# Kernel tuning notes

Measured on AMD Instinct MI355X. Metric: run time of the kernel, lower is better.

The kernel has to match this reference:

```python
import jax, jax.numpy as jnp
import numpy as np

B, N, D = 16, 2048, 128  # batch, nodes, embedding_dim

def setup_inputs() -> dict:
    key = jax.random.key(0)
    ks = jax.random.split(key, 12)
    def dense(kw, kb, din, dout):
        # keras Dense default glorot_uniform weight, zeros bias (use small random bias for generality)
        lim = np.sqrt(6.0 / (din + dout))
        W = jax.random.uniform(kw, (din, dout), minval=-lim, maxval=lim, dtype=jnp.float32)
        b = jax.random.normal(kb, (dout,), dtype=jnp.float32) * 0.01
        return W, b
    Wq, bq = dense(ks[0], ks[1], D, D)
    Wk, bk = dense(ks[2], ks[3], D, D)
    Wv, bv = dense(ks[4], ks[5], D, D)
    Wo, bo = dense(ks[6], ks[7], D, D)
    query_ = jax.random.normal(ks[8], (B, N, D), dtype=jnp.float32)
    key_ = jax.random.normal(ks[9], (B, N, D), dtype=jnp.float32)
    mask = jax.random.randint(ks[10], (B, N + 1, N + 1), 0, 2).astype(bool)
    return {"query_": query_, "key_": key_, "mask": mask,
            "Wq": Wq, "bq": bq, "Wk": Wk, "bk": bk,
            "Wv": Wv, "bv": bv, "Wo": Wo, "bo": bo}

def reference(query_, key_, mask, Wq, bq, Wk, bk, Wv, bv, Wo, bo):
    q = query_ @ Wq + bq                       # [B,N,D]
    k = key_ @ Wk + bk                         # [B,N,D]
    comp = jnp.einsum('bqd,bkd->bqk', q, k)    # [B,N,N]
    comp = comp / jnp.sqrt(jnp.asarray(k.shape[-1], jnp.float32))
    m = mask[:, 1:, 1:]                        # [B,N,N]
    comp = jnp.where(m, -jnp.inf, comp)
    attn = jax.nn.softmax(comp, axis=-1)
    attn = jnp.where(jnp.isnan(attn), 0.0, attn)  # fully-masked rows -> 0
    # NOTE: faithful to source: value projection applied to the PROJECTED key
    v = k @ Wv + bv                            # [B,N,D]
    out = jnp.einsum('bqk,bkd->bqd', attn, v)
    return out @ Wo + bo
```

## Files before the change

### kernel.cpp

```cpp
#include <hip/hip_runtime.h>

#define SB 16
#define SN 2048
#define SD 128
#define NM 2049
#define SZ (SB*SN*SD)

typedef __bf16 bf16x8 __attribute__((ext_vector_type(8)));
typedef float f32x4 __attribute__((ext_vector_type(4)));

__device__ __forceinline__ unsigned short f2b(float f){
  union { float f; unsigned int u; } v; v.f = f;
  unsigned int r = v.u + 0x7fffu + ((v.u >> 16) & 1u);
  return (unsigned short)(r >> 16);
}

__device__ __forceinline__ void async16(const void* g, void* l){
  __builtin_amdgcn_global_load_lds(
      (__attribute__((address_space(1))) void*)(g),
      (__attribute__((address_space(3))) void*)(l), 16, 0, 0);
}

__global__ __launch_bounds__(256) void prep_w_kernel(
    const float* __restrict__ Wq, const float* __restrict__ Wk,
    const float* __restrict__ Wv, const float* __restrict__ Wo,
    unsigned short* __restrict__ out)
{
  int widx = blockIdx.x >> 4;
  int kg   = blockIdx.x & 15;
  const float* W = (widx==0)?Wq:(widx==1)?Wk:(widx==2)?Wv:Wo;
  unsigned short* O = out + widx*16384;
  int t = threadIdx.x;
  int k = kg*8 + (t>>5);
  int n = (t&31)*4;
  float4 v = *reinterpret_cast<const float4*>(W + k*SD + n);
  O[(n+0)*SD + k] = f2b(v.x);
  O[(n+1)*SD + k] = f2b(v.y);
  O[(n+2)*SD + k] = f2b(v.z);
  O[(n+3)*SD + k] = f2b(v.w);
}

__global__ __launch_bounds__(256,4) void qkv_kernel(
    const float* __restrict__ query, const float* __restrict__ key,
    const unsigned short* __restrict__ wts,
    const float* __restrict__ bq, const float* __restrict__ bk,
    const float* __restrict__ bv,
    unsigned short* __restrict__ qb, unsigned short* __restrict__ kb,
    unsigned short* __restrict__ vt)
{
  __shared__ unsigned short kstrip[2][16*136];
  __shared__ unsigned short vT[SD*40];

  int tid=threadIdx.x;
  int w=tid>>6, ln=tid&63, g=ln>>4, lm=ln&15;
  int b = blockIdx.x >> 6, nt = blockIdx.x & 63;
  int n0 = nt*32;
  size_t rowbase = (size_t)b*SN + n0;
  const float sc = 0.08838834764831845f;

  const unsigned short* WqT = wts;
  const unsigned short* WkT = wts + 16384;
  const unsigned short* WvT = wts + 32768;

  if (w < 2){
    const float* xr = query + (rowbase + w*16 + lm)*SD;
    bf16x8 af[4];
    for (int ks=0;ks<4;ks++){
      float4 x0 = *reinterpret_cast<const float4*>(xr + ks*32 + g*8);
      float4 x1 = *reinterpret_cast<const float4*>(xr + ks*32 + g*8 + 4);
      union { bf16x8 v; unsigned short s[8]; } u;
      u.s[0]=f2b(x0.x); u.s[1]=f2b(x0.y); u.s[2]=f2b(x0.z); u.s[3]=f2b(x0.w);
      u.s[4]=f2b(x1.x); u.s[5]=f2b(x1.y); u.s[6]=f2b(x1.z); u.s[7]=f2b(x1.w);
      af[ks]=u.v;
    }
    for (int d=0; d<8; d++){
      f32x4 acc = {0.f,0.f,0.f,0.f};
      for (int ks=0;ks<4;ks++){
        bf16x8 wf = *reinterpret_cast<const bf16x8*>(WqT + (d*16+lm)*SD + ks*32 + g*8);
        acc = __builtin_amdgcn_mfma_f32_16x16x32_bf16(af[ks], wf, acc, 0,0,0);
      }
      float bb = bq[d*16+lm];
      for (int r=0;r<4;r++)
        qb[(rowbase + w*16 + 4*g + r)*SD + d*16 + lm] = f2b((acc[r]+bb)*sc);
    }
  } else {
    int wv = w-2;
    const float* xr = key + (rowbase + wv*16 + lm)*SD;
    bf16x8 af[4];
    for (int ks=0;ks<4;ks++){
      float4 x0 = *reinterpret_cast<const float4*>(xr + ks*32 + g*8);
      float4 x1 = *reinterpret_cast<const float4*>(xr + ks*32 + g*8 + 4);
      union { bf16x8 v; unsigned short s[8]; } u;
      u.s[0]=f2b(x0.x); u.s[1]=f2b(x0.y); u.s[2]=f2b(x0.z); u.s[3]=f2b(x0.w);
      u.s[4]=f2b(x1.x); u.s[5]=f2b(x1.y); u.s[6]=f2b(x1.z); u.s[7]=f2b(x1.w);
      af[ks]=u.v;
    }
    unsigned short* ks_ = kstrip[wv];
    for (int d=0; d<8; d++){
      f32x4 acc = {0.f,0.f,0.f,0.f};
      for (int ks=0;ks<4;ks++){
        bf16x8 wf = *reinterpret_cast<const bf16x8*>(WkT + (d*16+lm)*SD + ks*32 + g*8);
        acc = __builtin_amdgcn_mfma_f32_16x16x32_bf16(af[ks], wf, acc, 0,0,0);
      }
      float bb = bk[d*16+lm];
      for (int r=0;r<4;r++){
        unsigned short kv = f2b(acc[r]+bb);
        kb[(rowbase + wv*16 + 4*g + r)*SD + d*16 + lm] = kv;
        ks_[(4*g+r)*136 + d*16 + lm] = kv;
      }
    }
    bf16x8 ka[4];
    for (int ks=0;ks<4;ks++)
      ka[ks] = *reinterpret_cast<const bf16x8*>(&ks_[lm*136 + ks*32 + g*8]);
    for (int d=0; d<8; d++){
      f32x4 acc = {0.f,0.f,0.f,0.f};
      for (int ks=0;ks<4;ks++){
        bf16x8 wf = *reinterpret_cast<const bf16x8*>(WvT + (d*16+lm)*SD + ks*32 + g*8);
        acc = __builtin_amdgcn_mfma_f32_16x16x32_bf16(ka[ks], wf, acc, 0,0,0);
      }
      float bb = bv[d*16+lm];
      ushort4 pk;
      pk.x=f2b(acc[0]+bb); pk.y=f2b(acc[1]+bb);
      pk.z=f2b(acc[2]+bb); pk.w=f2b(acc[3]+bb);
      *reinterpret_cast<ushort4*>(&vT[(d*16+lm)*40 + wv*16 + 4*g]) = pk;
    }
  }
  __syncthreads();
  int d = tid>>1, half = tid&1;
  const uint4* src = reinterpret_cast<const uint4*>(&vT[d*40 + half*16]);
  uint4* dst = reinterpret_cast<uint4*>(vt + (size_t)b*SD*SN + (size_t)d*SN + n0 + half*16);
  dst[0]=src[0]; dst[1]=src[1];
}

__global__ __launch_bounds__(256,4) void flash_kernel(
    const unsigned short* __restrict__ qb, const unsigned short* __restrict__ kb,
    const unsigned short* __restrict__ vt, const int* __restrict__ mask,
    const unsigned short* __restrict__ WoT, const float* __restrict__ bo,
    float* __restrict__ out)
{
  __shared__ unsigned short bufK[2][64*128];
  __shared__ unsigned short bufV[2][128*64];
  __shared__ unsigned short ldsP[4*16*72];

  int tid=threadIdx.x;
  int w=tid>>6, ln=tid&63, g=ln>>4, lm=ln&15;
  int b = blockIdx.x >> 5, qt = blockIdx.x & 31;
  int q0 = qt*64;

  const unsigned short* Qb = qb + (size_t)b*SN*SD;
  const unsigned short* Kb = kb + (size_t)b*SN*SD;
  const unsigned short* Vb = vt + (size_t)b*SD*SN;
  const int* Mb = mask + (size_t)b*NM*NM;

  auto issueK = [&](int k0, int bi){
    const char* gbase = (const char*)Kb + (size_t)k0*256;
    for (int c=0;c<4;c++){
      int p = c*256 + tid;
      int row = p>>4, lc = (p&15) ^ (row&15);
      async16(gbase + (size_t)row*256 + lc*16, (char*)bufK[bi] + p*16);
    }
  };
  auto issueV = [&](int k0, int bi){
    const char* gbase = (const char*)Vb + (size_t)k0*2;
    for (int c=0;c<4;c++){
      int p = c*256 + tid;
      int row = p>>3, lc = (p&7) ^ (row&7);
      async16(gbase + (size_t)row*4096 + lc*16, (char*)bufV[bi] + p*16);
    }
  };

  issueK(0,0); issueV(0,0);

  bf16x8 qf[4];
  {
    const unsigned short* qr = Qb + (size_t)(q0 + w*16 + lm)*SD;
    for (int ks=0;ks<4;ks++)
      qf[ks] = *reinterpret_cast<const bf16x8*>(qr + ks*32 + g*8);
  }

  int qr1 = 1 + q0 + w*16 + 4*g;
  const int* mbase = Mb + (size_t)qr1*NM + 1 + lm;
  int mreg[16];
  for (int ct=0;ct<4;ct++)
    for (int r=0;r<4;r++)
      mreg[ct*4+r] = mbase[(size_t)r*NM + ct*16];

  float mrow[4], lrow[4], al[4];
  f32x4 acc[8];
  for (int r=0;r<4;r++){ mrow[r]=-INFINITY; lrow[r]=0.f; }
  for (int d=0;d<8;d++){ f32x4 z={0.f,0.f,0.f,0.f}; acc[d]=z; }
  unsigned short* pw = &ldsP[w*16*72];

  for (int kt=0; kt<32; kt++){
    __syncthreads();
    int cur = kt&1;
    if (kt<31){ issueK((kt+1)*64, cur^1); issueV((kt+1)*64, cur^1); }

    f32x4 s[4];
    for (int ct=0;ct<4;ct++){
      f32x4 z = {0.f,0.f,0.f,0.f};
      for (int ks=0;ks<4;ks++){
        bf16x8 kf = *reinterpret_cast<const bf16x8*>(
            &bufK[cur][(ct*16+lm)*128 + (((ks*4+g)^lm))*8]);
        z = __builtin_amdgcn_mfma_f32_16x16x32_bf16(qf[ks], kf, z, 0,0,0);
      }
      s[ct]=z;
    }

    for (int ct=0;ct<4;ct++)
      for (int r=0;r<4;r++)
        s[ct][r] = mreg[ct*4+r] ? -INFINITY : s[ct][r];
    if (kt<31){
      const int* mp = mbase + (kt+1)*64;
      for (int ct=0;ct<4;ct++)
        for (int r=0;r<4;r++)
          mreg[ct*4+r] = mp[(size_t)r*NM + ct*16];
    }

    for (int r=0;r<4;r++){
      float v = fmaxf(fmaxf(s[0][r],s[1][r]), fmaxf(s[2][r],s[3][r]));
      v = fmaxf(v, __shfl_xor(v,1,16));
      v = fmaxf(v, __shfl_xor(v,2,16));
      v = fmaxf(v, __shfl_xor(v,4,16));
      v = fmaxf(v, __shfl_xor(v,8,16));
      float mn = fmaxf(mrow[r], v);
      bool dead = (mn == -INFINITY);
      float a = dead ? 1.f : __expf(mrow[r]-mn);
      float rsum = 0.f;
      for (int ct=0;ct<4;ct++){
        float p = dead ? 0.f : __expf(s[ct][r]-mn);
        s[ct][r]=p; rsum += p;
      }
      rsum += __shfl_xor(rsum,1,16);
      rsum += __shfl_xor(rsum,2,16);
      rsum += __shfl_xor(rsum,4,16);
      rsum += __shfl_xor(rsum,8,16);
      lrow[r] = lrow[r]*a + rsum;
      mrow[r] = mn;
      al[r] = a;
    }
    for (int d=0;d<8;d++)
      for (int r=0;r<4;r++)
        acc[d][r] *= al[r];

    for (int ct=0;ct<4;ct++){
      int col = ct*16+lm;
      for (int r=0;r<4;r++)
        pw[(4*g+r)*72 + col] = f2b(s[ct][r]);
    }
    bf16x8 pa0 = *reinterpret_cast<const bf16x8*>(&pw[lm*72 + g*8]);
    bf16x8 pa1 = *reinterpret_cast<const bf16x8*>(&pw[lm*72 + 32 + g*8]);

    for (int d=0;d<8;d++){
      bf16x8 v0 = *reinterpret_cast<const bf16x8*>(
          &bufV[cur][(d*16+lm)*64 + ((g^(lm&7)))*8]);
      acc[d] = __builtin_amdgcn_mfma_f32_16x16x32_bf16(pa0, v0, acc[d], 0,0,0);
      bf16x8 v1 = *reinterpret_cast<const bf16x8*>(
          &bufV[cur][(d*16+lm)*64 + (((4+g)^(lm&7)))*8]);
      acc[d] = __builtin_amdgcn_mfma_f32_16x16x32_bf16(pa1, v1, acc[d], 0,0,0);
    }
  }

  __syncthreads();
  float inv[4];
  for (int r=0;r<4;r++) inv[r] = (lrow[r] > 0.f) ? (1.f/lrow[r]) : 0.f;
  unsigned short* strip = &bufK[0][0] + w*2176;
  for (int d=0;d<8;d++)
    for (int r=0;r<4;r++)
      strip[(4*g+r)*136 + d*16 + lm] = f2b(acc[d][r]*inv[r]);
  bf16x8 oa[4];
  for (int ks=0;ks<4;ks++)
    oa[ks] = *reinterpret_cast<const bf16x8*>(&strip[lm*136 + ks*32 + g*8]);
  float* Ob = out + ((size_t)b*SN + q0 + w*16)*SD;
  for (int dc=0; dc<8; dc++){
    f32x4 o = {0.f,0.f,0.f,0.f};
    for (int ks=0;ks<4;ks++){
      bf16x8 wf = *reinterpret_cast<const bf16x8*>(WoT + (dc*16+lm)*SD + ks*32 + g*8);
      o = __builtin_amdgcn_mfma_f32_16x16x32_bf16(oa[ks], wf, o, 0,0,0);
    }
    float bb = bo[dc*16+lm];
    for (int r=0;r<4;r++)
      Ob[(size_t)(4*g+r)*SD + dc*16 + lm] = o[r]+bb;
  }
}

extern "C" void kernel_launch(void* const* d_in, const int* in_sizes, int n_in,
                              void* d_out, int out_size, void* d_ws, size_t ws_size,
                              hipStream_t stream)
{
  const float* query = (const float*)d_in[0];
  const float* key   = (const float*)d_in[1];
  const int*   mask  = (const int*)d_in[2];
  const float* Wq = (const float*)d_in[3];
  const float* bq = (const float*)d_in[4];
  const float* Wk = (const float*)d_in[5];
  const float* bk = (const float*)d_in[6];
  const float* Wv = (const float*)d_in[7];
  const float* bv = (const float*)d_in[8];
  const float* Wo = (const float*)d_in[9];
  const float* bo = (const float*)d_in[10];
  float* out = (float*)d_out;

  unsigned short* qb = (unsigned short*)d_ws;
  unsigned short* kb = qb + SZ;
  unsigned short* vt = kb + SZ;
  unsigned short* wts = vt + SZ;

  prep_w_kernel<<<64,256,0,stream>>>(Wq,Wk,Wv,Wo,wts);
  qkv_kernel  <<<1024,256,0,stream>>>(query, key, wts, bq, bk, bv, qb, kb, vt);
  flash_kernel<<<512,256,0,stream>>>(qb, kb, vt, mask, wts+49152, bo, out);
}
```

Baseline: 490.7 us.

## Pre-pack mask into bitmasks and stage QKV weights in LDS

Adds a pre-pass that converts the int32 mask into 64-bit ballot bitmasks per row and key tile, so the flash kernel reads one 8-byte word per row per tile instead of sixteen scattered int loads. The QKV kernel is restructured to split Q and K/V blocks, stage the bf16 weight matrices in padded LDS, and write V transposed in wider chunks. Probabilities use a cheaper round-to-nearest bf16 conversion. This trades an extra full pass over the mask for smaller, coalesced mask reads inside the attention loop, and it uses more LDS per block in the QKV kernel.

```diff
diff --git a/kernel.cpp b/kernel.cpp
--- a/kernel.cpp
+++ b/kernel.cpp
@@ -5,6 +5,7 @@
 #define SD 128
 #define NM 2049
 #define SZ (SB*SN*SD)
+#define WLDS 17408
 
 typedef __bf16 bf16x8 __attribute__((ext_vector_type(8)));
 typedef float f32x4 __attribute__((ext_vector_type(4)));
@@ -14,6 +15,10 @@
   unsigned int r = v.u + 0x7fffu + ((v.u >> 16) & 1u);
   return (unsigned short)(r >> 16);
 }
+__device__ __forceinline__ unsigned short f2b_fast(float f){
+  union { float f; unsigned int u; } v; v.f = f;
+  return (unsigned short)((v.u + 0x8000u) >> 16);
+}
 
 __device__ __forceinline__ void async16(const void* g, void* l){
   __builtin_amdgcn_global_load_lds(
@@ -21,26 +26,52 @@
       (__attribute__((address_space(3))) void*)(l), 16, 0, 0);
 }
 
-__global__ __launch_bounds__(256) void prep_w_kernel(
+__global__ __launch_bounds__(256) void prep_pack_kernel(
     const float* __restrict__ Wq, const float* __restrict__ Wk,
     const float* __restrict__ Wv, const float* __restrict__ Wo,
-    unsigned short* __restrict__ out)
+    const int* __restrict__ mask,
+    unsigned short* __restrict__ wts, unsigned long long* __restrict__ pm)
 {
-  int widx = blockIdx.x >> 4;
-  int kg   = blockIdx.x & 15;
-  const float* W = (widx==0)?Wq:(widx==1)?Wk:(widx==2)?Wv:Wo;
-  unsigned short* O = out + widx*16384;
-  int t = threadIdx.x;
-  int k = kg*8 + (t>>5);
-  int n = (t&31)*4;
-  float4 v = *reinterpret_cast<const float4*>(W + k*SD + n);
-  O[(n+0)*SD + k] = f2b(v.x);
-  O[(n+1)*SD + k] = f2b(v.y);
-  O[(n+2)*SD + k] = f2b(v.z);
-  O[(n+3)*SD + k] = f2b(v.w);
-}
-
-__global__ __launch_bounds__(256,4) void qkv_kernel(
+  if (blockIdx.x < 64){
+    int widx = blockIdx.x >> 4;
+    int kg   = blockIdx.x & 15;
+    const float* W = (widx==0)?Wq:(widx==1)?Wk:(widx==2)?Wv:Wo;
+    unsigned short* O = wts + widx*16384;
+    int t = threadIdx.x;
+    int k = kg*8 + (t>>5);
+    int n = (t&31)*4;
+    float4 v = *reinterpret_cast<const float4*>(W + k*SD + n);
+    O[(n+0)*SD + k] = f2b(v.x);
+    O[(n+1)*SD + k] = f2b(v.y);
+    O[(n+2)*SD + k] = f2b(v.z);
+    O[(n+3)*SD + k] = f2b(v.w);
+    return;
+  }
+  int widx = blockIdx.x - 64;
+  int wave = widx*4 + (threadIdx.x>>6);
+  int ln = threadIdx.x & 63;
+  size_t wb0 = (size_t)wave*256;
+  for (int rr=0; rr<32; rr++){
+    size_t wb = wb0 + rr*8;
+    int v[8];
+    for (int i=0;i<8;i++){
+      size_t wbi = wb + i;
+      int bb = (int)(wbi>>16); int rem = (int)(wbi & 65535);
+      int row = rem>>5; int kt = rem&31;
+      v[i] = mask[(size_t)bb*NM*NM + (size_t)(row+1)*NM + 1 + kt*64 + ln];
+    }
+    unsigned long long bt[8];
+    for (int i=0;i<8;i++) bt[i] = __ballot(v[i]!=0);
+    if (ln==0){
+      for (int i=0;i<4;i++){
+        ulonglong2 t; t.x = bt[2*i]; t.y = bt[2*i+1];
+        *reinterpret_cast<ulonglong2*>(&pm[wb + 2*i]) = t;
+      }
+    }
+  }
+}
+
+__global__ __launch_bounds__(256) void qkv_kernel(
     const float* __restrict__ query, const float* __restrict__ key,
     const unsigned short* __restrict__ wts,
     const float* __restrict__ bq, const float* __restrict__ bk,
@@ -48,22 +79,25 @@
     unsigned short* __restrict__ qb, unsigned short* __restrict__ kb,
     unsigned short* __restrict__ vt)
 {
-  __shared__ unsigned short kstrip[2][16*136];
-  __shared__ unsigned short vT[SD*40];
-
+  __shared__ unsigned short lds[2*WLDS + 9216];
   int tid=threadIdx.x;
   int w=tid>>6, ln=tid&63, g=ln>>4, lm=ln&15;
-  int b = blockIdx.x >> 6, nt = blockIdx.x & 63;
-  int n0 = nt*32;
-  size_t rowbase = (size_t)b*SN + n0;
+  bool isq = blockIdx.x < 512;
+  int id = isq ? blockIdx.x : (blockIdx.x - 512);
+  int bb = id>>5, n0 = (id&31)*64;
+  size_t rowbase = (size_t)bb*SN + n0 + w*16;
   const float sc = 0.08838834764831845f;
 
-  const unsigned short* WqT = wts;
-  const unsigned short* WkT = wts + 16384;
-  const unsigned short* WvT = wts + 32768;
-
-  if (w < 2){
-    const float* xr = query + (rowbase + w*16 + lm)*SD;
+  if (isq){
+    for (int i=0;i<8;i++){
+      int p = i*256+tid; int row=p>>4, c=p&15;
+      uint4 t = *reinterpret_cast<const uint4*>(wts + p*8);
+      *reinterpret_cast<uint4*>(&lds[row*136 + c*8]) = t;
+    }
+    __syncthreads();
+    float bqv[8];
+    for (int d=0;d<8;d++) bqv[d] = bq[d*16+lm];
+    const float* xr = query + (rowbase + lm)*SD;
     bf16x8 af[4];
     for (int ks=0;ks<4;ks++){
       float4 x0 = *reinterpret_cast<const float4*>(xr + ks*32 + g*8);
@@ -76,16 +110,27 @@
     for (int d=0; d<8; d++){
       f32x4 acc = {0.f,0.f,0.f,0.f};
       for (int ks=0;ks<4;ks++){
-        bf16x8 wf = *reinterpret_cast<const bf16x8*>(WqT + (d*16+lm)*SD + ks*32 + g*8);
+        bf16x8 wf = *reinterpret_cast<const bf16x8*>(&lds[(d*16+lm)*136 + ks*32 + g*8]);
         acc = __builtin_amdgcn_mfma_f32_16x16x32_bf16(af[ks], wf, acc, 0,0,0);
       }
-      float bb = bq[d*16+lm];
       for (int r=0;r<4;r++)
-        qb[(rowbase + w*16 + 4*g + r)*SD + d*16 + lm] = f2b((acc[r]+bb)*sc);
+        qb[(rowbase + 4*g + r)*SD + d*16 + lm] = f2b((acc[r]+bqv[d])*sc);
     }
   } else {
-    int wv = w-2;
-    const float* xr = key + (rowbase + wv*16 + lm)*SD;
+    for (int i=0;i<8;i++){
+      int p = i*256+tid; int row=p>>4, c=p&15;
+      uint4 t = *reinterpret_cast<const uint4*>(wts + 16384 + p*8);
+      *reinterpret_cast<uint4*>(&lds[row*136 + c*8]) = t;
+    }
+    for (int i=0;i<8;i++){
+      int p = i*256+tid; int row=p>>4, c=p&15;
+      uint4 t = *reinterpret_cast<const uint4*>(wts + 32768 + p*8);
+      *reinterpret_cast<uint4*>(&lds[WLDS + row*136 + c*8]) = t;
+    }
+    __syncthreads();
+    float bkv[8], bvv[8];
+    for (int d=0;d<8;d++){ bkv[d]=bk[d*16+lm]; bvv[d]=bv[d*16+lm]; }
+    const float* xr = key + (rowbase + lm)*SD;
     bf16x8 af[4];
     for (int ks=0;ks<4;ks++){
       float4 x0 = *reinterpret_cast<const float4*>(xr + ks*32 + g*8);
@@ -95,46 +140,47 @@
       u.s[4]=f2b(x1.x); u.s[5]=f2b(x1.y); u.s[6]=f2b(x1.z); u.s[7]=f2b(x1.w);
       af[ks]=u.v;
     }
-    unsigned short* ks_ = kstrip[wv];
+    unsigned short* strip = &lds[2*WLDS + w*2176];
     for (int d=0; d<8; d++){
       f32x4 acc = {0.f,0.f,0.f,0.f};
       for (int ks=0;ks<4;ks++){
-        bf16x8 wf = *reinterpret_cast<const bf16x8*>(WkT + (d*16+lm)*SD + ks*32 + g*8);
+        bf16x8 wf = *reinterpret_cast<const bf16x8*>(&lds[(d*16+lm)*136 + ks*32 + g*8]);
         acc = __builtin_amdgcn_mfma_f32_16x16x32_bf16(af[ks], wf, acc, 0,0,0);
       }
-      float bb = bk[d*16+lm];
       for (int r=0;r<4;r++){
-        unsigned short kv = f2b(acc[r]+bb);
-        kb[(rowbase + wv*16 + 4*g + r)*SD + d*16 + lm] = kv;
-        ks_[(4*g+r)*136 + d*16 + lm] = kv;
+        unsigned short kv2 = f2b(acc[r]+bkv[d]);
+        kb[(rowbase + 4*g + r)*SD + d*16 + lm] = kv2;
+        strip[(4*g+r)*136 + d*16 + lm] = kv2;
       }
     }
     bf16x8 ka[4];
     for (int ks=0;ks<4;ks++)
-      ka[ks] = *reinterpret_cast<const bf16x8*>(&ks_[lm*136 + ks*32 + g*8]);
+      ka[ks] = *reinterpret_cast<const bf16x8*>(&strip[lm*136 + ks*32 + g*8]);
+    __syncthreads();
+    unsigned short* vT = &lds[2*WLDS];
     for (int d=0; d<8; d++){
       f32x4 acc = {0.f,0.f,0.f,0.f};
       for (int ks=0;ks<4;ks++){
-        bf16x8 wf = *reinterpret_cast<const bf16x8*>(WvT + (d*16+lm)*SD + ks*32 + g*8);
+        bf16x8 wf = *reinterpret_cast<const bf16x8*>(&lds[WLDS + (d*16+lm)*136 + ks*32 + g*8]);
         acc = __builtin_amdgcn_mfma_f32_16x16x32_bf16(ka[ks], wf, acc, 0,0,0);
       }
-      float bb = bv[d*16+lm];
       ushort4 pk;
-      pk.x=f2b(acc[0]+bb); pk.y=f2b(acc[1]+bb);
-      pk.z=f2b(acc[2]+bb); pk.w=f2b(acc[3]+bb);
-      *reinterpret_cast<ushort4*>(&vT[(d*16+lm)*40 + wv*16 + 4*g]) = pk;
-    }
-  }
-  __syncthreads();
-  int d = tid>>1, half = tid&1;
-  const uint4* src = reinterpret_cast<const uint4*>(&vT[d*40 + half*16]);
-  uint4* dst = reinterpret_cast<uint4*>(vt + (size_t)b*SD*SN + (size_t)d*SN + n0 + half*16);
-  dst[0]=src[0]; dst[1]=src[1];
+      pk.x=f2b(acc[0]+bvv[d]); pk.y=f2b(acc[1]+bvv[d]);
+      pk.z=f2b(acc[2]+bvv[d]); pk.w=f2b(acc[3]+bvv[d]);
+      *reinterpret_cast<ushort4*>(&vT[(d*16+lm)*72 + w*16 + 4*g]) = pk;
+    }
+    __syncthreads();
+    for (int i=0;i<4;i++){
+      int idx = i*256+tid; int row = idx>>3, c8 = idx&7;
+      uint4 t = *reinterpret_cast<const uint4*>(&vT[row*72 + c8*8]);
+      *reinterpret_cast<uint4*>(vt + (size_t)bb*SD*SN + (size_t)row*SN + n0 + c8*8) = t;
+    }
+  }
 }
 
 __global__ __launch_bounds__(256,4) void flash_kernel(
     const unsigned short* __restrict__ qb, const unsigned short* __restrict__ kb,
-    const unsigned short* __restrict__ vt, const int* __restrict__ mask,
+    const unsigned short* __restrict__ vt, const unsigned long long* __restrict__ pm,
     const unsigned short* __restrict__ WoT, const float* __restrict__ bo,
     float* __restrict__ out)
 {
@@ -150,7 +196,6 @@
   const unsigned short* Qb = qb + (size_t)b*SN*SD;
   const unsigned short* Kb = kb + (size_t)b*SN*SD;
   const unsigned short* Vb = vt + (size_t)b*SD*SN;
-  const int* Mb = mask + (size_t)b*NM*NM;
 
   auto issueK = [&](int k0, int bi){
     const char* gbase = (const char*)Kb + (size_t)k0*256;
@@ -178,12 +223,9 @@
       qf[ks] = *reinterpret_cast<const bf16x8*>(qr + ks*32 + g*8);
   }
 
-  int qr1 = 1 + q0 + w*16 + 4*g;
-  const int* mbase = Mb + (size_t)qr1*NM + 1 + lm;
-  int mreg[16];
-  for (int ct=0;ct<4;ct++)
-    for (int r=0;r<4;r++)
-      mreg[ct*4+r] = mbase[(size_t)r*NM + ct*16];
+  const unsigned long long* pmr = pm + ((size_t)b*SN + q0 + w*16 + 4*g)*32;
+  unsigned long long pmc[4];
+  for (int r=0;r<4;r++) pmc[r] = pmr[(size_t)r*32];
 
   float mrow[4], lrow[4], al[4];
   f32x4 acc[8];
@@ -207,15 +249,17 @@
       s[ct]=z;
     }
 
-    for (int ct=0;ct<4;ct++)
-      for (int r=0;r<4;r++)
-        s[ct][r] = mreg[ct*4+r] ? -INFINITY : s[ct][r];
-    if (kt<31){
-      const int* mp = mbase + (kt+1)*64;
-      for (int ct=0;ct<4;ct++)
-        for (int r=0;r<4;r++)
-          mreg[ct*4+r] = mp[(size_t)r*NM + ct*16];
-    }
+    for (int r=0;r<4;r++){
+      unsigned int lo = (unsigned int)pmc[r];
+      unsigned int hi = (unsigned int)(pmc[r]>>32);
+      unsigned int l = lo >> lm, h = hi >> lm;
+      if (l & 1u)       s[0][r] = -INFINITY;
+      if (l & 0x10000u) s[1][r] = -INFINITY;
+      if (h & 1u)       s[2][r] = -INFINITY;
+      if (h & 0x10000u) s[3][r] = -INFINITY;
+    }
+    if (kt<31)
+      for (int r=0;r<4;r++) pmc[r] = pmr[(size_t)r*32 + kt + 1];
 
     for (int r=0;r<4;r++){
       float v = fmaxf(fmaxf(s[0][r],s[1][r]), fmaxf(s[2][r],s[3][r]));
@@ -246,7 +290,7 @@
     for (int ct=0;ct<4;ct++){
       int col = ct*16+lm;
       for (int r=0;r<4;r++)
-        pw[(4*g+r)*72 + col] = f2b(s[ct][r]);
+        pw[(4*g+r)*72 + col] = f2b_fast(s[ct][r]);
     }
     bf16x8 pa0 = *reinterpret_cast<const bf16x8*>(&pw[lm*72 + g*8]);
     bf16x8 pa1 = *reinterpret_cast<const bf16x8*>(&pw[lm*72 + 32 + g*8]);
@@ -305,8 +349,9 @@
   unsigned short* kb = qb + SZ;
   unsigned short* vt = kb + SZ;
   unsigned short* wts = vt + SZ;
-
-  prep_w_kernel<<<64,256,0,stream>>>(Wq,Wk,Wv,Wo,wts);
-  qkv_kernel  <<<1024,256,0,stream>>>(query, key, wts, bq, bk, bv, qb, kb, vt);
-  flash_kernel<<<512,256,0,stream>>>(qb, kb, vt, mask, wts+49152, bo, out);
-}
+  unsigned long long* pm = (unsigned long long*)(wts + 65536);
+
+  prep_pack_kernel<<<1088,256,0,stream>>>(Wq,Wk,Wv,Wo, mask, wts, pm);
+  qkv_kernel      <<<1024,256,0,stream>>>(query, key, wts, bq, bk, bv, qb, kb, vt);
+  flash_kernel    <<<512,256,0,stream>>>(qb, kb, vt, pm, wts+49152, bo, out);
+}
```

After: 519.7 us. +5.9%, slower.

## Pack int mask into bitmask in projection kernel; coalesce Q/K stores via LDS

Applied to the files above, without the earlier changes.

Adds 1024 extra blocks to the QKV projection kernel that read the int32 mask and ballot it into 64-bit bitmasks, one word per row per 64-column tile. The flash kernel then loads only these packed bits instead of strided int32 mask reads in its inner loop. Q and K outputs are now staged through LDS and written as 16-byte vectors, and P uses a cheaper rounding conversion. The mask still has to be read once in full, plus a write and re-read of the packed form, and the cheaper rounding slightly changes how ties round.

```diff
diff --git a/kernel.cpp b/kernel.cpp
--- a/kernel.cpp
+++ b/kernel.cpp
@@ -14,6 +14,10 @@
   unsigned int r = v.u + 0x7fffu + ((v.u >> 16) & 1u);
   return (unsigned short)(r >> 16);
 }
+__device__ __forceinline__ unsigned short f2b_fast(float f){
+  union { float f; unsigned int u; } v; v.f = f;
+  return (unsigned short)((v.u + 0x8000u) >> 16);
+}
 
 __device__ __forceinline__ void async16(const void* g, void* l){
   __builtin_amdgcn_global_load_lds(
@@ -24,117 +28,141 @@
 __global__ __launch_bounds__(256) void prep_w_kernel(
     const float* __restrict__ Wq, const float* __restrict__ Wk,
     const float* __restrict__ Wv, const float* __restrict__ Wo,
-    unsigned short* __restrict__ out)
+    unsigned short* __restrict__ wts)
 {
-  int widx = blockIdx.x >> 4;
-  int kg   = blockIdx.x & 15;
-  const float* W = (widx==0)?Wq:(widx==1)?Wk:(widx==2)?Wv:Wo;
-  unsigned short* O = out + widx*16384;
-  int t = threadIdx.x;
-  int k = kg*8 + (t>>5);
-  int n = (t&31)*4;
-  float4 v = *reinterpret_cast<const float4*>(W + k*SD + n);
-  O[(n+0)*SD + k] = f2b(v.x);
-  O[(n+1)*SD + k] = f2b(v.y);
-  O[(n+2)*SD + k] = f2b(v.z);
-  O[(n+3)*SD + k] = f2b(v.w);
-}
-
-__global__ __launch_bounds__(256,4) void qkv_kernel(
+  int widx=blockIdx.x>>4, kg=blockIdx.x&15;
+  const float* W=(widx==0)?Wq:(widx==1)?Wk:(widx==2)?Wv:Wo;
+  unsigned short* O=wts+widx*16384;
+  int t=threadIdx.x;
+  int k=kg*8+(t>>5), n=(t&31)*4;
+  float4 v=*reinterpret_cast<const float4*>(W+k*SD+n);
+  O[(n+0)*SD+k]=f2b(v.x); O[(n+1)*SD+k]=f2b(v.y);
+  O[(n+2)*SD+k]=f2b(v.z); O[(n+3)*SD+k]=f2b(v.w);
+}
+
+__global__ __launch_bounds__(256) void combo_kernel(
     const float* __restrict__ query, const float* __restrict__ key,
+    const int* __restrict__ mask,
     const unsigned short* __restrict__ wts,
     const float* __restrict__ bq, const float* __restrict__ bk,
     const float* __restrict__ bv,
     unsigned short* __restrict__ qb, unsigned short* __restrict__ kb,
-    unsigned short* __restrict__ vt)
+    unsigned short* __restrict__ vt, unsigned long long* __restrict__ pm)
 {
-  __shared__ unsigned short kstrip[2][16*136];
-  __shared__ unsigned short vT[SD*40];
-
+  __shared__ unsigned short smem[13824];
   int tid=threadIdx.x;
   int w=tid>>6, ln=tid&63, g=ln>>4, lm=ln&15;
-  int b = blockIdx.x >> 6, nt = blockIdx.x & 63;
-  int n0 = nt*32;
-  size_t rowbase = (size_t)b*SN + n0;
-  const float sc = 0.08838834764831845f;
-
-  const unsigned short* WqT = wts;
-  const unsigned short* WkT = wts + 16384;
-  const unsigned short* WvT = wts + 32768;
+
+  if (blockIdx.x >= 1024){
+    int widx = blockIdx.x - 1024;
+    int wave = widx*4 + w;
+    size_t wb0=(size_t)wave*256;
+    for (int rr=0; rr<32; rr++){
+      size_t wb=wb0+rr*8;
+      int v[8];
+      for (int i=0;i<8;i++){
+        size_t wbi=wb+i;
+        int grow=(int)(wbi>>5), kt=(int)(wbi&31);
+        int bb=grow>>11, brow=grow&2047;
+        v[i]=mask[(size_t)bb*NM*NM+(size_t)(brow+1)*NM+1+kt*64+ln];
+      }
+      unsigned long long bt[8];
+      for (int i=0;i<8;i++) bt[i]=__ballot(v[i]!=0);
+      if (ln==0){
+        for (int i=0;i<4;i++){
+          ulonglong2 t; t.x=bt[2*i]; t.y=bt[2*i+1];
+          *reinterpret_cast<ulonglong2*>(&pm[wb+2*i])=t;
+        }
+      }
+    }
+    return;
+  }
+
+  int id=blockIdx.x;
+  int b=id>>6, nt=id&63, n0=nt*32;
+  const float sc=0.08838834764831845f;
+  unsigned short* strip = smem + w*2176;
+  unsigned short* vT    = smem + 8704;
 
   if (w < 2){
-    const float* xr = query + (rowbase + w*16 + lm)*SD;
+    size_t rowq=(size_t)b*SN+n0+w*16;
+    const float* xr=query+(rowq+lm)*SD;
     bf16x8 af[4];
     for (int ks=0;ks<4;ks++){
-      float4 x0 = *reinterpret_cast<const float4*>(xr + ks*32 + g*8);
-      float4 x1 = *reinterpret_cast<const float4*>(xr + ks*32 + g*8 + 4);
+      float4 x0=*reinterpret_cast<const float4*>(xr+ks*32+g*8);
+      float4 x1=*reinterpret_cast<const float4*>(xr+ks*32+g*8+4);
       union { bf16x8 v; unsigned short s[8]; } u;
       u.s[0]=f2b(x0.x); u.s[1]=f2b(x0.y); u.s[2]=f2b(x0.z); u.s[3]=f2b(x0.w);
       u.s[4]=f2b(x1.x); u.s[5]=f2b(x1.y); u.s[6]=f2b(x1.z); u.s[7]=f2b(x1.w);
       af[ks]=u.v;
     }
-    for (int d=0; d<8; d++){
-      f32x4 acc = {0.f,0.f,0.f,0.f};
+    for (int d=0;d<8;d++){
+      f32x4 acc={0.f,0.f,0.f,0.f};
       for (int ks=0;ks<4;ks++){
-        bf16x8 wf = *reinterpret_cast<const bf16x8*>(WqT + (d*16+lm)*SD + ks*32 + g*8);
-        acc = __builtin_amdgcn_mfma_f32_16x16x32_bf16(af[ks], wf, acc, 0,0,0);
-      }
-      float bb = bq[d*16+lm];
+        bf16x8 wf=*reinterpret_cast<const bf16x8*>(wts+(d*16+lm)*SD+ks*32+g*8);
+        acc=__builtin_amdgcn_mfma_f32_16x16x32_bf16(af[ks],wf,acc,0,0,0);
+      }
+      float bb2=bq[d*16+lm];
       for (int r=0;r<4;r++)
-        qb[(rowbase + w*16 + 4*g + r)*SD + d*16 + lm] = f2b((acc[r]+bb)*sc);
+        strip[(4*g+r)*136+d*16+lm]=f2b((acc[r]+bb2)*sc);
+    }
+    for (int ks=0;ks<4;ks++){
+      bf16x8 qfr=*reinterpret_cast<const bf16x8*>(&strip[lm*136+ks*32+g*8]);
+      *reinterpret_cast<bf16x8*>(qb+(rowq+lm)*SD+ks*32+g*8)=qfr;
     }
   } else {
-    int wv = w-2;
-    const float* xr = key + (rowbase + wv*16 + lm)*SD;
+    int wv=w-2;
+    size_t rowk=(size_t)b*SN+n0+wv*16;
+    const float* xr=key+(rowk+lm)*SD;
     bf16x8 af[4];
     for (int ks=0;ks<4;ks++){
-      float4 x0 = *reinterpret_cast<const float4*>(xr + ks*32 + g*8);
-      float4 x1 = *reinterpret_cast<const float4*>(xr + ks*32 + g*8 + 4);
+      float4 x0=*reinterpret_cast<const float4*>(xr+ks*32+g*8);
+      float4 x1=*reinterpret_cast<const float4*>(xr+ks*32+g*8+4);
       union { bf16x8 v; unsigned short s[8]; } u;
       u.s[0]=f2b(x0.x); u.s[1]=f2b(x0.y); u.s[2]=f2b(x0.z); u.s[3]=f2b(x0.w);
       u.s[4]=f2b(x1.x); u.s[5]=f2b(x1.y); u.s[6]=f2b(x1.z); u.s[7]=f2b(x1.w);
       af[ks]=u.v;
     }
-    unsigned short* ks_ = kstrip[wv];
-    for (int d=0; d<8; d++){
-      f32x4 acc = {0.f,0.f,0.f,0.f};
+    for (int d=0;d<8;d++){
+      f32x4 acc={0.f,0.f,0.f,0.f};
       for (int ks=0;ks<4;ks++){
-        bf16x8 wf = *reinterpret_cast<const bf16x8*>(WkT + (d*16+lm)*SD + ks*32 + g*8);
-        acc = __builtin_amdgcn_mfma_f32_16x16x32_bf16(af[ks], wf, acc, 0,0,0);
-      }
-      float bb = bk[d*16+lm];
-      for (int r=0;r<4;r++){
-        unsigned short kv = f2b(acc[r]+bb);
-        kb[(rowbase + wv*16 + 4*g + r)*SD + d*16 + lm] = kv;
-        ks_[(4*g+r)*136 + d*16 + lm] = kv;
-      }
+        bf16x8 wf=*reinterpret_cast<const bf16x8*>(wts+16384+(d*16+lm)*SD+ks*32+g*8);
+        acc=__builtin_amdgcn_mfma_f32_16x16x32_bf16(af[ks],wf,acc,0,0,0);
+      }
+      float bb2=bk[d*16+lm];
+      for (int r=0;r<4;r++)
+        strip[(4*g+r)*136+d*16+lm]=f2b(acc[r]+bb2);
     }
     bf16x8 ka[4];
-    for (int ks=0;ks<4;ks++)
-      ka[ks] = *reinterpret_cast<const bf16x8*>(&ks_[lm*136 + ks*32 + g*8]);
-    for (int d=0; d<8; d++){
-      f32x4 acc = {0.f,0.f,0.f,0.f};
+    for (int ks=0;ks<4;ks++){
+      ka[ks]=*reinterpret_cast<const bf16x8*>(&strip[lm*136+ks*32+g*8]);
+      *reinterpret_cast<bf16x8*>(kb+(rowk+lm)*SD+ks*32+g*8)=ka[ks];
+    }
+    for (int d=0;d<8;d++){
+      f32x4 acc={0.f,0.f,0.f,0.f};
       for (int ks=0;ks<4;ks++){
-        bf16x8 wf = *reinterpret_cast<const bf16x8*>(WvT + (d*16+lm)*SD + ks*32 + g*8);
-        acc = __builtin_amdgcn_mfma_f32_16x16x32_bf16(ka[ks], wf, acc, 0,0,0);
-      }
-      float bb = bv[d*16+lm];
+        bf16x8 wf=*reinterpret_cast<const bf16x8*>(wts+32768+(d*16+lm)*SD+ks*32+g*8);
+        acc=__builtin_amdgcn_mfma_f32_16x16x32_bf16(ka[ks],wf,acc,0,0,0);
+      }
+      float bb2=bv[d*16+lm];
       ushort4 pk;
-      pk.x=f2b(acc[0]+bb); pk.y=f2b(acc[1]+bb);
-      pk.z=f2b(acc[2]+bb); pk.w=f2b(acc[3]+bb);
-      *reinterpret_cast<ushort4*>(&vT[(d*16+lm)*40 + wv*16 + 4*g]) = pk;
+      pk.x=f2b(acc[0]+bb2); pk.y=f2b(acc[1]+bb2);
+      pk.z=f2b(acc[2]+bb2); pk.w=f2b(acc[3]+bb2);
+      *reinterpret_cast<ushort4*>(&vT[(d*16+lm)*40+wv*16+4*g])=pk;
     }
   }
   __syncthreads();
-  int d = tid>>1, half = tid&1;
-  const uint4* src = reinterpret_cast<const uint4*>(&vT[d*40 + half*16]);
-  uint4* dst = reinterpret_cast<uint4*>(vt + (size_t)b*SD*SN + (size_t)d*SN + n0 + half*16);
-  dst[0]=src[0]; dst[1]=src[1];
+  {
+    int d=tid>>1, half=tid&1;
+    const uint4* src=reinterpret_cast<const uint4*>(&vT[d*40+half*16]);
+    uint4* dst=reinterpret_cast<uint4*>(vt+(size_t)b*SD*SN+(size_t)d*SN+n0+half*16);
+    dst[0]=src[0]; dst[1]=src[1];
+  }
 }
 
 __global__ __launch_bounds__(256,4) void flash_kernel(
     const unsigned short* __restrict__ qb, const unsigned short* __restrict__ kb,
-    const unsigned short* __restrict__ vt, const int* __restrict__ mask,
+    const unsigned short* __restrict__ vt, const unsigned long long* __restrict__ pm,
     const unsigned short* __restrict__ WoT, const float* __restrict__ bo,
     float* __restrict__ out)
 {
@@ -150,22 +178,21 @@
   const unsigned short* Qb = qb + (size_t)b*SN*SD;
   const unsigned short* Kb = kb + (size_t)b*SN*SD;
   const unsigned short* Vb = vt + (size_t)b*SD*SN;
-  const int* Mb = mask + (size_t)b*NM*NM;
 
   auto issueK = [&](int k0, int bi){
-    const char* gbase = (const char*)Kb + (size_t)k0*256;
+    const char* gbase=(const char*)Kb+(size_t)k0*256;
     for (int c=0;c<4;c++){
-      int p = c*256 + tid;
-      int row = p>>4, lc = (p&15) ^ (row&15);
-      async16(gbase + (size_t)row*256 + lc*16, (char*)bufK[bi] + p*16);
+      int p=c*256+tid;
+      int row=p>>4, lc=(p&15)^(row&15);
+      async16(gbase+(size_t)row*256+lc*16, (char*)bufK[bi]+p*16);
     }
   };
   auto issueV = [&](int k0, int bi){
-    const char* gbase = (const char*)Vb + (size_t)k0*2;
+    const char* gbase=(const char*)Vb+(size_t)k0*2;
     for (int c=0;c<4;c++){
-      int p = c*256 + tid;
-      int row = p>>3, lc = (p&7) ^ (row&7);
-      async16(gbase + (size_t)row*4096 + lc*16, (char*)bufV[bi] + p*16);
+      int p=c*256+tid;
+      int row=p>>3, lc=(p&7)^(row&7);
+      async16(gbase+(size_t)row*4096+lc*16, (char*)bufV[bi]+p*16);
     }
   };
 
@@ -178,109 +205,108 @@
       qf[ks] = *reinterpret_cast<const bf16x8*>(qr + ks*32 + g*8);
   }
 
-  int qr1 = 1 + q0 + w*16 + 4*g;
-  const int* mbase = Mb + (size_t)qr1*NM + 1 + lm;
-  int mreg[16];
-  for (int ct=0;ct<4;ct++)
-    for (int r=0;r<4;r++)
-      mreg[ct*4+r] = mbase[(size_t)r*NM + ct*16];
+  const unsigned long long* pmr = pm + ((size_t)b*SN + q0 + w*16 + 4*g)*32;
+  unsigned long long pmc[4];
+  for (int r=0;r<4;r++) pmc[r]=pmr[(size_t)r*32];
 
   float mrow[4], lrow[4], al[4];
   f32x4 acc[8];
   for (int r=0;r<4;r++){ mrow[r]=-INFINITY; lrow[r]=0.f; }
   for (int d=0;d<8;d++){ f32x4 z={0.f,0.f,0.f,0.f}; acc[d]=z; }
-  unsigned short* pw = &ldsP[w*16*72];
+  unsigned short* pw=&ldsP[w*1152];
 
   for (int kt=0; kt<32; kt++){
     __syncthreads();
-    int cur = kt&1;
+    int cur=kt&1;
     if (kt<31){ issueK((kt+1)*64, cur^1); issueV((kt+1)*64, cur^1); }
 
     f32x4 s[4];
     for (int ct=0;ct<4;ct++){
-      f32x4 z = {0.f,0.f,0.f,0.f};
+      f32x4 z={0.f,0.f,0.f,0.f};
       for (int ks=0;ks<4;ks++){
-        bf16x8 kf = *reinterpret_cast<const bf16x8*>(
+        bf16x8 kf=*reinterpret_cast<const bf16x8*>(
             &bufK[cur][(ct*16+lm)*128 + (((ks*4+g)^lm))*8]);
-        z = __builtin_amdgcn_mfma_f32_16x16x32_bf16(qf[ks], kf, z, 0,0,0);
+        z=__builtin_amdgcn_mfma_f32_16x16x32_bf16(qf[ks],kf,z,0,0,0);
       }
       s[ct]=z;
     }
 
-    for (int ct=0;ct<4;ct++)
-      for (int r=0;r<4;r++)
-        s[ct][r] = mreg[ct*4+r] ? -INFINITY : s[ct][r];
-    if (kt<31){
-      const int* mp = mbase + (kt+1)*64;
-      for (int ct=0;ct<4;ct++)
-        for (int r=0;r<4;r++)
-          mreg[ct*4+r] = mp[(size_t)r*NM + ct*16];
-    }
-
     for (int r=0;r<4;r++){
-      float v = fmaxf(fmaxf(s[0][r],s[1][r]), fmaxf(s[2][r],s[3][r]));
-      v = fmaxf(v, __shfl_xor(v,1,16));
-      v = fmaxf(v, __shfl_xor(v,2,16));
-      v = fmaxf(v, __shfl_xor(v,4,16));
-      v = fmaxf(v, __shfl_xor(v,8,16));
-      float mn = fmaxf(mrow[r], v);
-      bool dead = (mn == -INFINITY);
-      float a = dead ? 1.f : __expf(mrow[r]-mn);
-      float rsum = 0.f;
+      unsigned int lo=(unsigned int)pmc[r];
+      unsigned int hi=(unsigned int)(pmc[r]>>32);
+      unsigned int l=lo>>lm, h=hi>>lm;
+      if (l & 1u)       s[0][r]=-INFINITY;
+      if (l & 0x10000u) s[1][r]=-INFINITY;
+      if (h & 1u)       s[2][r]=-INFINITY;
+      if (h & 0x10000u) s[3][r]=-INFINITY;
+    }
+    if (kt<31)
+      for (int r=0;r<4;r++) pmc[r]=pmr[(size_t)r*32+kt+1];
+
+    for (int r=0;r<4;r++){
+      float v=fmaxf(fmaxf(s[0][r],s[1][r]),fmaxf(s[2][r],s[3][r]));
+      v=fmaxf(v,__shfl_xor(v,1,16));
+      v=fmaxf(v,__shfl_xor(v,2,16));
+      v=fmaxf(v,__shfl_xor(v,4,16));
+      v=fmaxf(v,__shfl_xor(v,8,16));
+      float mn=fmaxf(mrow[r],v);
+      bool dead=(mn==-INFINITY);
+      float a=dead?1.f:__expf(mrow[r]-mn);
+      float rsum=0.f;
       for (int ct=0;ct<4;ct++){
-        float p = dead ? 0.f : __expf(s[ct][r]-mn);
-        s[ct][r]=p; rsum += p;
-      }
-      rsum += __shfl_xor(rsum,1,16);
-      rsum += __shfl_xor(rsum,2,16);
-      rsum += __shfl_xor(rsum,4,16);
-      rsum += __shfl_xor(rsum,8,16);
-      lrow[r] = lrow[r]*a + rsum;
-      mrow[r] = mn;
-      al[r] = a;
+        float p=dead?0.f:__expf(s[ct][r]-mn);
+        s[ct][r]=p; rsum+=p;
+      }
+      rsum+=__shfl_xor(rsum,1,16);
+      rsum+=__shfl_xor(rsum,2,16);
+      rsum+=__shfl_xor(rsum,4,16);
+      rsum+=__shfl_xor(rsum,8,16);
+      lrow[r]=lrow[r]*a+rsum;
+      mrow[r]=mn;
+      al[r]=a;
     }
     for (int d=0;d<8;d++)
       for (int r=0;r<4;r++)
-        acc[d][r] *= al[r];
+        acc[d][r]*=al[r];
 
     for (int ct=0;ct<4;ct++){
-      int col = ct*16+lm;
+      int col=ct*16+lm;
       for (int r=0;r<4;r++)
-        pw[(4*g+r)*72 + col] = f2b(s[ct][r]);
-    }
-    bf16x8 pa0 = *reinterpret_cast<const bf16x8*>(&pw[lm*72 + g*8]);
-    bf16x8 pa1 = *reinterpret_cast<const bf16x8*>(&pw[lm*72 + 32 + g*8]);
+        pw[(4*g+r)*72+col]=f2b_fast(s[ct][r]);
+    }
+    bf16x8 pa0=*reinterpret_cast<const bf16x8*>(&pw[lm*72+g*8]);
+    bf16x8 pa1=*reinterpret_cast<const bf16x8*>(&pw[lm*72+32+g*8]);
 
     for (int d=0;d<8;d++){
-      bf16x8 v0 = *reinterpret_cast<const bf16x8*>(
+      bf16x8 v0=*reinterpret_cast<const bf16x8*>(
           &bufV[cur][(d*16+lm)*64 + ((g^(lm&7)))*8]);
-      acc[d] = __builtin_amdgcn_mfma_f32_16x16x32_bf16(pa0, v0, acc[d], 0,0,0);
-      bf16x8 v1 = *reinterpret_cast<const bf16x8*>(
+      acc[d]=__builtin_amdgcn_mfma_f32_16x16x32_bf16(pa0,v0,acc[d],0,0,0);
+      bf16x8 v1=*reinterpret_cast<const bf16x8*>(
           &bufV[cur][(d*16+lm)*64 + (((4+g)^(lm&7)))*8]);
-      acc[d] = __builtin_amdgcn_mfma_f32_16x16x32_bf16(pa1, v1, acc[d], 0,0,0);
+      acc[d]=__builtin_amdgcn_mfma_f32_16x16x32_bf16(pa1,v1,acc[d],0,0,0);
     }
   }
 
   __syncthreads();
   float inv[4];
-  for (int r=0;r<4;r++) inv[r] = (lrow[r] > 0.f) ? (1.f/lrow[r]) : 0.f;
-  unsigned short* strip = &bufK[0][0] + w*2176;
+  for (int r=0;r<4;r++) inv[r]=(lrow[r]>0.f)?(1.f/lrow[r]):0.f;
+  unsigned short* estrip = &bufK[0][0] + w*2176;
   for (int d=0;d<8;d++)
     for (int r=0;r<4;r++)
-      strip[(4*g+r)*136 + d*16 + lm] = f2b(acc[d][r]*inv[r]);
+      estrip[(4*g+r)*136+d*16+lm]=f2b(acc[d][r]*inv[r]);
   bf16x8 oa[4];
   for (int ks=0;ks<4;ks++)
-    oa[ks] = *reinterpret_cast<const bf16x8*>(&strip[lm*136 + ks*32 + g*8]);
+    oa[ks]=*reinterpret_cast<const bf16x8*>(&estrip[lm*136+ks*32+g*8]);
   float* Ob = out + ((size_t)b*SN + q0 + w*16)*SD;
-  for (int dc=0; dc<8; dc++){
-    f32x4 o = {0.f,0.f,0.f,0.f};
-    for (int ks=0;ks<4;ks++){
-      bf16x8 wf = *reinterpret_cast<const bf16x8*>(WoT + (dc*16+lm)*SD + ks*32 + g*8);
-      o = __builtin_amdgcn_mfma_f32_16x16x32_bf16(oa[ks], wf, o, 0,0,0);
-    }
-    float bb = bo[dc*16+lm];
+  for (int dc=0;dc<8;dc++){
+    f32x4 o={0.f,0.f,0.f,0.f};
+    for (int ks=0;ks<4;ks++){
+      bf16x8 wf=*reinterpret_cast<const bf16x8*>(WoT+(dc*16+lm)*SD+ks*32+g*8);
+      o=__builtin_amdgcn_mfma_f32_16x16x32_bf16(oa[ks],wf,o,0,0,0);
+    }
+    float bb2=bo[dc*16+lm];
     for (int r=0;r<4;r++)
-      Ob[(size_t)(4*g+r)*SD + dc*16 + lm] = o[r]+bb;
+      Ob[(size_t)(4*g+r)*SD+dc*16+lm]=o[r]+bb2;
   }
 }
 
@@ -288,25 +314,26 @@
                               void* d_out, int out_size, void* d_ws, size_t ws_size,
                               hipStream_t stream)
 {
-  const float* query = (const float*)d_in[0];
-  const float* key   = (const float*)d_in[1];
-  const int*   mask  = (const int*)d_in[2];
-  const float* Wq = (const float*)d_in[3];
-  const float* bq = (const float*)d_in[4];
-  const float* Wk = (const float*)d_in[5];
-  const float* bk = (const float*)d_in[6];
-  const float* Wv = (const float*)d_in[7];
-  const float* bv = (const float*)d_in[8];
-  const float* Wo = (const float*)d_in[9];
-  const float* bo = (const float*)d_in[10];
-  float* out = (float*)d_out;
-
-  unsigned short* qb = (unsigned short*)d_ws;
-  unsigned short* kb = qb + SZ;
-  unsigned short* vt = kb + SZ;
-  unsigned short* wts = vt + SZ;
+  const float* query=(const float*)d_in[0];
+  const float* key  =(const float*)d_in[1];
+  const int*   mask =(const int*)d_in[2];
+  const float* Wq=(const float*)d_in[3];
+  const float* bq=(const float*)d_in[4];
+  const float* Wk=(const float*)d_in[5];
+  const float* bk=(const float*)d_in[6];
+  const float* Wv=(const float*)d_in[7];
+  const float* bv=(const float*)d_in[8];
+  const float* Wo=(const float*)d_in[9];
+  const float* bo=(const float*)d_in[10];
+  float* out=(float*)d_out;
+
+  unsigned short* qb=(unsigned short*)d_ws;
+  unsigned short* kb=qb+SZ;
+  unsigned short* vt=kb+SZ;
+  unsigned short* wts=vt+SZ;
+  unsigned long long* pm=(unsigned long long*)(wts+65536);
 
   prep_w_kernel<<<64,256,0,stream>>>(Wq,Wk,Wv,Wo,wts);
-  qkv_kernel  <<<1024,256,0,stream>>>(query, key, wts, bq, bk, bv, qb, kb, vt);
-  flash_kernel<<<512,256,0,stream>>>(qb, kb, vt, mask, wts+49152, bo, out);
-}
+  combo_kernel <<<2048,256,0,stream>>>(query,key,mask,wts,bq,bk,bv,qb,kb,vt,pm);
+  flash_kernel <<<512,256,0,stream>>>(qb,kb,vt,pm,wts+49152,bo,out);
+}
```

After: 527.0 us. 7.4% more time.
